# Optimization experiments

Hardware: AMD Instinct MI355X
Metric: run time of the kernel (lower is better)

Reference implementation:

```python
import jax, jax.numpy as jnp
import numpy as np

B, NF, NI = 4, 8, 1
C_ASPP = 512
H32, W32 = 32, 32
H8, W8 = 128, 128
C = C_ASPP // 16  # 32 channels after PixelShuffle(4)
D = 32 * 4 + 4 * 1 + 4 + 1  # 137 dynamic-kernel params per instance
BN_EPS = 1e-5


def pixel_shuffle(x, r):
    # torch PixelShuffle: out[n, c, h*r+i, w*r+j] = in[n, c*r*r + i*r + j, h, w]
    n, cr2, h, w = x.shape
    c = cr2 // (r * r)
    x = x.reshape(n, c, r, r, h, w)
    x = x.transpose(0, 1, 4, 2, 5, 3)
    return x.reshape(n, c, h * r, w * r)


def conv2d(x, w, b, pad):
    y = jax.lax.conv_general_dilated(
        x, w, window_strides=(1, 1), padding=[(pad, pad), (pad, pad)],
        dimension_numbers=("NCHW", "OIHW", "NCHW"))
    return y + b[None, :, None, None]


def setup_inputs() -> dict:
    key = jax.random.key(0)
    ks = jax.random.split(key, 6)
    return {
        "embedding": jax.random.normal(ks[0], (B * NF, C_ASPP, H32, W32), jnp.float32),
        "inc_kernels": jax.random.normal(ks[1], (B, NF, NI, D), jnp.float32) * 0.1,
        "coarse_masks": jax.random.uniform(ks[2], (B, NF, NI, H8, W8), dtype=jnp.float32),
        "conv_w": jax.random.normal(ks[3], (C, C, 3, 3), jnp.float32) * 0.05,
        "conv_b": jnp.zeros((C,), jnp.float32),
        "bn_gamma": jnp.ones((C,), jnp.float32),
        "bn_beta": jnp.zeros((C,), jnp.float32),
        "bn_mean": jnp.zeros((C,), jnp.float32),
        "bn_var": jnp.ones((C,), jnp.float32),
        "smooth_w": jax.random.normal(ks[4], (1, 2, 5, 5), jnp.float32) * 0.05,
        "smooth_b": jnp.zeros((1,), jnp.float32),
    }


def reference(embedding, inc_kernels, coarse_masks, conv_w, conv_b,
              bn_gamma, bn_beta, bn_mean, bn_var, smooth_w, smooth_b):
    # inc_conv: PixelShuffle(4) -> Conv3x3 -> BatchNorm(eval) -> ReLU
    x = pixel_shuffle(embedding, 4)              # (B*NF, 32, 128, 128)
    x = conv2d(x, conv_w, conv_b, 1)
    scale = (bn_gamma / jnp.sqrt(bn_var + BN_EPS))[None, :, None, None]
    x = (x - bn_mean[None, :, None, None]) * scale + bn_beta[None, :, None, None]
    x = jax.nn.relu(x)

    # per-instance dynamic 1x1 convs (groups = B*NF*NI; NI=1 so each frame is a group)
    G = B * NF * NI
    k = inc_kernels.reshape(G, D)
    w1 = k[:, :128].reshape(G, 4, 32)            # layer1: 32 -> 4
    w2 = k[:, 128:132].reshape(G, 1, 4)          # layer2: 4 -> 1
    b1 = k[:, 132:136]
    b2 = k[:, 136:137]

    hfeat = jax.nn.relu(jnp.einsum('goc,gchw->gohw', w1, x) + b1[:, :, None, None])
    y = jnp.einsum('goc,gchw->gohw', w2, hfeat) + b2[:, :, None, None]  # (G,1,H8,W8)

    m = coarse_masks.reshape(G, 1, H8, W8)
    z = jnp.concatenate([jax.nn.sigmoid(y), m], axis=1)  # (G, 2, H8, W8)
    z = conv2d(z, smooth_w, smooth_b, 2)                 # inc_smooth 5x5
    return z.reshape(B * NF, NI, H8, W8)
```

## Files before the change

kernel.cpp:

```cpp
#include <hip/hip_runtime.h>


typedef __attribute__((ext_vector_type(8))) short short8;
typedef __attribute__((ext_vector_type(4))) float f32x4;

static __device__ __forceinline__ ushort f2bf(float x) {
    union { float f; uint u; } v; v.f = x;
    uint r = v.u + 0x7fffu + ((v.u >> 16) & 1u);
    return (ushort)(r >> 16);
}
static __device__ __forceinline__ uint cvt_pk_bf16(float lo, float hi) {
    uint r;
    asm("v_cvt_pk_bf16_f32 %0, %1, %2" : "=v"(r) : "v"(lo), "v"(hi));
    return r;
}

#define SIG_ELEMS (32 * 128 * 128)
#define BFRAG_OFF (SIG_ELEMS * 4)
#define SH_OFF    (BFRAG_OFF + 18432)
#define HDP_OFF   (SH_OFF + 128)

__global__ void prep_kernel(const float* __restrict__ conv_w,
                            const float* __restrict__ conv_b,
                            const float* __restrict__ bn_gamma,
                            const float* __restrict__ bn_beta,
                            const float* __restrict__ bn_mean,
                            const float* __restrict__ bn_var,
                            const float* __restrict__ inc,
                            ushort* __restrict__ bfrag,
                            float* __restrict__ shb,
                            float* __restrict__ hdp) {
    int t = blockIdx.x * 256 + threadIdx.x;
    if (t < 9216) {
        int j    = t & 7;
        int lane = (t >> 3) & 63;
        int knt  = t >> 9;
        int kk   = knt >> 1;
        int nt   = knt & 1;
        int oc   = (lane & 15) + nt * 16;
        int c    = (lane >> 4) * 8 + j;
        float sc = bn_gamma[oc] * rsqrtf(bn_var[oc] + 1e-5f);
        bfrag[t] = f2bf(conv_w[oc * 288 + c * 9 + kk] * sc);
    } else if (t < 9248) {
        int oc = t - 9216;
        float sc = bn_gamma[oc] * rsqrtf(bn_var[oc] + 1e-5f);
        shb[oc] = (conv_b[oc] - bn_mean[oc]) * sc + bn_beta[oc];
    } else if (t < 9248 + 32 * 137) {
        int i = t - 9248;
        int nn = i / 137, r = i - nn * 137;
        hdp[nn * 144 + r] = inc[i];
    }
}

#define PITCHB 8320
#define NRING  6

__global__ __launch_bounds__(256, 2) void fused_main_kernel(
    const float* __restrict__ emb,
    const ushort* __restrict__ bfrag,
    const float* __restrict__ shb,
    const float* __restrict__ hdp,
    float* __restrict__ sig_out)
{
    __shared__ __align__(16) char smem[NRING * PITCHB];

    const int bid = blockIdx.x;
    const int lid = (bid & 7) * 64 + (bid >> 3);
    const int n   = lid >> 4;
    const int q   = lid & 15;
    const int hq0 = q << 3;

    const int tid  = threadIdx.x;

    const int f    = tid & 7;
    const int cphi = (tid >> 3) & 3;
    const int sx   = (tid >> 5) & 3;
    const int yy   = tid >> 7;

    {
        const int rA = yy, rB = yy + 2;
        const int hA = hq0 + rA - 1, hB = hq0 + rB - 1;
        const bool vA = (unsigned)hA < 128u;
        const bool vB = (unsigned)hB < 128u;
        float4 pA0[4], pA1[4], pB0[4], pB1[4];
        #pragma unroll
        for (int cplo = 0; cplo < 4; ++cplo) {
            pA0[cplo] = make_float4(0.f, 0.f, 0.f, 0.f);
            pA1[cplo] = pA0[cplo]; pB0[cplo] = pA0[cplo]; pB1[cplo] = pA0[cplo];
            if (vA) {
                int cc = cphi * 128 + cplo * 32 + ((hA & 3) << 2) + sx;
                long base = ((long)(n * 512 + cc) << 10) + ((hA >> 2) << 5) + (f << 2);
                pA0[cplo] = *reinterpret_cast<const float4*>(&emb[base]);
                pA1[cplo] = *reinterpret_cast<const float4*>(&emb[base + (16 << 10)]);
            }
            if (vB) {
                int cc = cphi * 128 + cplo * 32 + ((hB & 3) << 2) + sx;
                long base = ((long)(n * 512 + cc) << 10) + ((hB >> 2) << 5) + (f << 2);
                pB0[cplo] = *reinterpret_cast<const float4*>(&emb[base]);
                pB1[cplo] = *reinterpret_cast<const float4*>(&emb[base + (16 << 10)]);
            }
        }
        __builtin_amdgcn_sched_barrier(0);
        if (tid < 192) {
            int cell = tid >> 4;
            int wrd  = tid & 15;
            int row  = cell >> 1;
            int col  = (cell & 1) ? 129 : 0;
            ((uint*)smem)[(row * PITCHB + col * 64) / 4 + wrd] = 0u;
        }
        const float a00[4] = {pA0[0].x, pA0[0].y, pA0[0].z, pA0[0].w};
        const float a01[4] = {pA0[1].x, pA0[1].y, pA0[1].z, pA0[1].w};
        const float a02[4] = {pA0[2].x, pA0[2].y, pA0[2].z, pA0[2].w};
        const float a03[4] = {pA0[3].x, pA0[3].y, pA0[3].z, pA0[3].w};
        const float a10[4] = {pA1[0].x, pA1[0].y, pA1[0].z, pA1[0].w};
        const float a11[4] = {pA1[1].x, pA1[1].y, pA1[1].z, pA1[1].w};
        const float a12[4] = {pA1[2].x, pA1[2].y, pA1[2].z, pA1[2].w};
        const float a13[4] = {pA1[3].x, pA1[3].y, pA1[3].z, pA1[3].w};
        const float b00[4] = {pB0[0].x, pB0[0].y, pB0[0].z, pB0[0].w};
        const float b01[4] = {pB0[1].x, pB0[1].y, pB0[1].z, pB0[1].w};
        const float b02[4] = {pB0[2].x, pB0[2].y, pB0[2].z, pB0[2].w};
        const float b03[4] = {pB0[3].x, pB0[3].y, pB0[3].z, pB0[3].w};
        const float b10[4] = {pB1[0].x, pB1[0].y, pB1[0].z, pB1[0].w};
        const float b11[4] = {pB1[1].x, pB1[1].y, pB1[1].z, pB1[1].w};
        const float b12[4] = {pB1[2].x, pB1[2].y, pB1[2].z, pB1[2].w};
        const float b13[4] = {pB1[3].x, pB1[3].y, pB1[3].z, pB1[3].w};
        #pragma unroll
        for (int e = 0; e < 4; ++e) {
            int xi   = 1 + sx + (f << 4) + (e << 2);
            int slot = (cphi ^ ((xi >> 1) ^ (xi >> 4))) & 3;
            int off  = xi * 64 + (slot << 4);
            uint4 qa;
            qa.x = cvt_pk_bf16(a00[e], a10[e]);
            qa.y = cvt_pk_bf16(a01[e], a11[e]);
            qa.z = cvt_pk_bf16(a02[e], a12[e]);
            qa.w = cvt_pk_bf16(a03[e], a13[e]);
            *reinterpret_cast<uint4*>(&smem[rA * PITCHB + off]) = qa;
            uint4 qb;
            qb.x = cvt_pk_bf16(b00[e], b10[e]);
            qb.y = cvt_pk_bf16(b01[e], b11[e]);
            qb.z = cvt_pk_bf16(b02[e], b12[e]);
            qb.w = cvt_pk_bf16(b03[e], b13[e]);
            *reinterpret_cast<uint4*>(&smem[rB * PITCHB + off]) = qb;
        }
    }

    const int lane = tid & 63;
    const int wv   = tid >> 6;
    const int g    = lane >> 4;
    const int m    = lane & 15;
    const int rw   = wv >> 1;
    const int xq   = (wv & 1) * 64;

    int cell_off[4][3];
    #pragma unroll
    for (int t = 0; t < 4; ++t)
        #pragma unroll
        for (int dx = 0; dx < 3; ++dx) {
            int xi = xq + t * 16 + m + dx;
            int slot = (g ^ ((xi >> 1) ^ (xi >> 4))) & 3;
            cell_off[t][dx] = xi * 64 + (slot << 4);
        }

    short8 bf0[9], bf1[9];
    #pragma unroll
    for (int kk = 0; kk < 9; ++kk) {
        bf0[kk] = *reinterpret_cast<const short8*>(bfrag + (((kk * 2 + 0) * 64 + lane) << 3));
        bf1[kk] = *reinterpret_cast<const short8*>(bfrag + (((kk * 2 + 1) * 64 + lane) << 3));
    }

    const float* hd = hdp + n * 144;
    const f32x4 shA = *reinterpret_cast<const f32x4*>(&shb[g * 4]);
    const f32x4 shB = *reinterpret_cast<const f32x4*>(&shb[16 + g * 4]);
    f32x4 w1A[4], w1B[4];
    #pragma unroll
    for (int o = 0; o < 4; ++o) {
        w1A[o] = *reinterpret_cast<const f32x4*>(&hd[o * 32 + g * 4]);
        w1B[o] = *reinterpret_cast<const f32x4*>(&hd[o * 32 + 16 + g * 4]);
    }
    const f32x4 w2v = *reinterpret_cast<const f32x4*>(&hd[128]);
    const f32x4 b1v = *reinterpret_cast<const f32x4*>(&hd[132]);
    const float b2  = hd[136];

    __syncthreads();

    #pragma unroll 1
    for (int it = 0; it < 4; ++it) {
        float4 np0[4], np1[4];
        const bool have = (it < 3);
        const int  hn   = hq0 + 2 * it + 3 + yy;
        const bool vn   = have && (hn < 128);
        #pragma unroll
        for (int cplo = 0; cplo < 4; ++cplo) {
            np0[cplo] = make_float4(0.f, 0.f, 0.f, 0.f);
            np1[cplo] = np0[cplo];
            if (vn) {
                int cc = cphi * 128 + cplo * 32 + ((hn & 3) << 2) + sx;
                long base = ((long)(n * 512 + cc) << 10) + ((hn >> 2) << 5) + (f << 2);
                np0[cplo] = *reinterpret_cast<const float4*>(&emb[base]);
                np1[cplo] = *reinterpret_cast<const float4*>(&emb[base + (16 << 10)]);
            }
        }
        __builtin_amdgcn_sched_barrier(0);

        int rb[3];
        #pragma unroll
        for (int dy = 0; dy < 3; ++dy) {
            int r = 2 * it + rw + dy;
            if (r >= NRING) r -= NRING;
            rb[dy] = r * PITCHB;
        }

        f32x4 acc[4][2];
        #pragma unroll
        for (int t = 0; t < 4; ++t)
            #pragma unroll
            for (int nt = 0; nt < 2; ++nt)
                acc[t][nt] = (f32x4){0.f, 0.f, 0.f, 0.f};

        __builtin_amdgcn_s_setprio(1);
        #pragma unroll
        for (int kk = 0; kk < 9; ++kk) {
            const int dy = kk / 3, dxs = kk % 3;
            #pragma unroll
            for (int t = 0; t < 4; ++t) {
                short8 a = *reinterpret_cast<const short8*>(&smem[rb[dy] + cell_off[t][dxs]]);
                acc[t][0] = __builtin_amdgcn_mfma_f32_16x16x32_bf16(bf0[kk], a, acc[t][0], 0, 0, 0);
                acc[t][1] = __builtin_amdgcn_mfma_f32_16x16x32_bf16(bf1[kk], a, acc[t][1], 0, 0, 0);
            }
        }
        __builtin_amdgcn_s_setprio(0);

        float ph[4][4];
        #pragma unroll
        for (int t = 0; t < 4; ++t) {
            f32x4 vA, vB;
            vA.x = fmaxf(acc[t][0].x + shA.x, 0.f);
            vA.y = fmaxf(acc[t][0].y + shA.y, 0.f);
            vA.z = fmaxf(acc[t][0].z + shA.z, 0.f);
            vA.w = fmaxf(acc[t][0].w + shA.w, 0.f);
            vB.x = fmaxf(acc[t][1].x + shB.x, 0.f);
            vB.y = fmaxf(acc[t][1].y + shB.y, 0.f);
            vB.z = fmaxf(acc[t][1].z + shB.z, 0.f);
            vB.w = fmaxf(acc[t][1].w + shB.w, 0.f);
            #pragma unroll
            for (int o = 0; o < 4; ++o) {
                float p = vA.x * w1A[o].x;
                p = fmaf(vA.y, w1A[o].y, p);
                p = fmaf(vA.z, w1A[o].z, p);
                p = fmaf(vA.w, w1A[o].w, p);
                p = fmaf(vB.x, w1B[o].x, p);
                p = fmaf(vB.y, w1B[o].y, p);
                p = fmaf(vB.z, w1B[o].z, p);
                p = fmaf(vB.w, w1B[o].w, p);
                ph[t][o] = p;
            }
        }
        #pragma unroll
        for (int t = 0; t < 4; ++t)
            #pragma unroll
            for (int o = 0; o < 4; ++o) {
                float s = ph[t][o];
                s += __shfl_xor(s, 16);
                s += __shfl_xor(s, 32);
                ph[t][o] = s;
            }
        float yv[4];
        #pragma unroll
        for (int t = 0; t < 4; ++t) {
            float q0 = fmaxf(ph[t][0] + b1v.x, 0.f);
            float q1 = fmaxf(ph[t][1] + b1v.y, 0.f);
            float q2 = fmaxf(ph[t][2] + b1v.z, 0.f);
            float q3 = fmaxf(ph[t][3] + b1v.w, 0.f);
            float yyv = b2;
            yyv = fmaf(w2v.x, q0, yyv);
            yyv = fmaf(w2v.y, q1, yyv);
            yyv = fmaf(w2v.z, q2, yyv);
            yyv = fmaf(w2v.w, q3, yyv);
            yv[t] = yyv;
        }
        float ysel = (g == 0) ? yv[0] : (g == 1) ? yv[1] : (g == 2) ? yv[2] : yv[3];
        float sv = 1.0f / (1.0f + __expf(-ysel));
        sig_out[(n << 14) + ((hq0 + 2 * it + rw) << 7) + xq + lane] = sv;

        if (have) {
            int rs = 2 * it + 4 + yy;
            if (rs >= NRING) rs -= NRING;
            const float c00[4] = {np0[0].x, np0[0].y, np0[0].z, np0[0].w};
            const float c01[4] = {np0[1].x, np0[1].y, np0[1].z, np0[1].w};
            const float c02[4] = {np0[2].x, np0[2].y, np0[2].z, np0[2].w};
            const float c03[4] = {np0[3].x, np0[3].y, np0[3].z, np0[3].w};
            const float c10[4] = {np1[0].x, np1[0].y, np1[0].z, np1[0].w};
            const float c11[4] = {np1[1].x, np1[1].y, np1[1].z, np1[1].w};
            const float c12[4] = {np1[2].x, np1[2].y, np1[2].z, np1[2].w};
            const float c13[4] = {np1[3].x, np1[3].y, np1[3].z, np1[3].w};
            #pragma unroll
            for (int e = 0; e < 4; ++e) {
                int xi   = 1 + sx + (f << 4) + (e << 2);
                int slot = (cphi ^ ((xi >> 1) ^ (xi >> 4))) & 3;
                uint4 qv;
                qv.x = cvt_pk_bf16(c00[e], c10[e]);
                qv.y = cvt_pk_bf16(c01[e], c11[e]);
                qv.z = cvt_pk_bf16(c02[e], c12[e]);
                qv.w = cvt_pk_bf16(c03[e], c13[e]);
                *reinterpret_cast<uint4*>(&smem[rs * PITCHB + xi * 64 + (slot << 4)]) = qv;
            }
        }
        __syncthreads();
    }
}

__global__ __launch_bounds__(256) void smooth_kernel(
    const float* __restrict__ sig,
    const float* __restrict__ masks,
    const float* __restrict__ sw,
    const float* __restrict__ sb,
    float* __restrict__ out)
{
    __shared__ float ls[2][400];

    const int tid  = threadIdx.x;
    const int n    = blockIdx.x >> 6;
    const int tile = blockIdx.x & 63;
    const int h0   = (tile >> 3) << 4;
    const int w0   = (tile & 7) << 4;

    for (int i = tid; i < 800; i += 256) {
        int chn = (i >= 400) ? 1 : 0;
        int r  = i - chn * 400;
        int yy = r / 20;
        int xx = r - yy * 20;
        int h  = h0 + yy - 2;
        int w  = w0 + xx - 2;
        float v = 0.0f;
        if ((unsigned)h < 128u && (unsigned)w < 128u) {
            const float* src = chn ? masks : sig;
            v = src[(n << 14) + (h << 7) + w];
        }
        ls[chn][r] = v;
    }
    __syncthreads();

    const int tx = tid & 15;
    const int ty = tid >> 4;

    float accv = sb[0];
    #pragma unroll
    for (int chn = 0; chn < 2; ++chn)
        #pragma unroll
        for (int dy = 0; dy < 5; ++dy)
            #pragma unroll
            for (int dx = 0; dx < 5; ++dx)
                accv = fmaf(ls[chn][(ty + dy) * 20 + tx + dx],
                            sw[(chn * 5 + dy) * 5 + dx], accv);
    out[(n << 14) + ((h0 + ty) << 7) + (w0 + tx)] = accv;
}

extern "C" void kernel_launch(void* const* d_in, const int* in_sizes, int n_in,
                              void* d_out, int out_size, void* d_ws, size_t ws_size,
                              hipStream_t stream) {
    const float* emb     = (const float*)d_in[0];
    const float* inc     = (const float*)d_in[1];
    const float* masks   = (const float*)d_in[2];
    const float* conv_w  = (const float*)d_in[3];
    const float* conv_b  = (const float*)d_in[4];
    const float* bn_g    = (const float*)d_in[5];
    const float* bn_b    = (const float*)d_in[6];
    const float* bn_m    = (const float*)d_in[7];
    const float* bn_v    = (const float*)d_in[8];
    const float* sw      = (const float*)d_in[9];
    const float* sb      = (const float*)d_in[10];
    float*  out   = (float*)d_out;
    float*  sig   = (float*)d_ws;
    ushort* bfrag = (ushort*)((char*)d_ws + BFRAG_OFF);
    float*  shb   = (float*)((char*)d_ws + SH_OFF);
    float*  hdp   = (float*)((char*)d_ws + HDP_OFF);

    prep_kernel<<<54, 256, 0, stream>>>(conv_w, conv_b, bn_g, bn_b, bn_m, bn_v,
                                        inc, bfrag, shb, hdp);
    fused_main_kernel<<<512, 256, 0, stream>>>(emb, bfrag, shb, hdp, sig);
    smooth_kernel<<<2048, 256, 0, stream>>>(sig, masks, sw, sb, out);
}
```

Baseline: 33.91 us.

## Halve rows per block, double grid, raise occupancy and cut shuffle reduction

Each block now handles 4 output rows instead of 8, so the grid doubles to 1024 blocks, and launch bounds allow 3 blocks per CU. The thread-to-load mapping is permuted so consecutive threads vary sx and cphi first. The per-pixel weight and shift loads move inside the loop to reduce register pressure. The cross-lane reduction becomes a butterfly exchange, cutting the shuffle count. The cost is a larger relative halo: each 4-row strip still loads 6 input rows, so redundant global reads and conversion work go up.

```diff
diff --git a/kernel.cpp b/kernel.cpp
--- a/kernel.cpp
+++ b/kernel.cpp
@@ -55,7 +55,7 @@
 #define PITCHB 8320
 #define NRING  6
 
-__global__ __launch_bounds__(256, 2) void fused_main_kernel(
+__global__ __launch_bounds__(256, 3) void fused_main_kernel(
     const float* __restrict__ emb,
     const ushort* __restrict__ bfrag,
     const float* __restrict__ shb,
@@ -65,16 +65,16 @@
     __shared__ __align__(16) char smem[NRING * PITCHB];
 
     const int bid = blockIdx.x;
-    const int lid = (bid & 7) * 64 + (bid >> 3);
-    const int n   = lid >> 4;
-    const int q   = lid & 15;
-    const int hq0 = q << 3;
+    const int lid = (bid & 7) * 128 + (bid >> 3);
+    const int n   = lid >> 5;
+    const int qc  = lid & 31;
+    const int hq0 = qc << 2;
 
     const int tid  = threadIdx.x;
 
-    const int f    = tid & 7;
-    const int cphi = (tid >> 3) & 3;
-    const int sx   = (tid >> 5) & 3;
+    const int sx   = tid & 3;
+    const int cphi = (tid >> 2) & 3;
+    const int f    = (tid >> 4) & 7;
     const int yy   = tid >> 7;
 
     {
@@ -150,6 +150,8 @@
     const int m    = lane & 15;
     const int rw   = wv >> 1;
     const int xq   = (wv & 1) * 64;
+    const int gb0  = g & 1;
+    const int gb1  = (g >> 1) & 1;
 
     int cell_off[4][3];
     #pragma unroll
@@ -169,14 +171,6 @@
     }
 
     const float* hd = hdp + n * 144;
-    const f32x4 shA = *reinterpret_cast<const f32x4*>(&shb[g * 4]);
-    const f32x4 shB = *reinterpret_cast<const f32x4*>(&shb[16 + g * 4]);
-    f32x4 w1A[4], w1B[4];
-    #pragma unroll
-    for (int o = 0; o < 4; ++o) {
-        w1A[o] = *reinterpret_cast<const f32x4*>(&hd[o * 32 + g * 4]);
-        w1B[o] = *reinterpret_cast<const f32x4*>(&hd[o * 32 + 16 + g * 4]);
-    }
     const f32x4 w2v = *reinterpret_cast<const f32x4*>(&hd[128]);
     const f32x4 b1v = *reinterpret_cast<const f32x4*>(&hd[132]);
     const float b2  = hd[136];
@@ -184,9 +178,9 @@
     __syncthreads();
 
     #pragma unroll 1
-    for (int it = 0; it < 4; ++it) {
+    for (int it = 0; it < 2; ++it) {
         float4 np0[4], np1[4];
-        const bool have = (it < 3);
+        const bool have = (it == 0);
         const int  hn   = hq0 + 2 * it + 3 + yy;
         const bool vn   = have && (hn < 128);
         #pragma unroll
@@ -204,11 +198,8 @@
 
         int rb[3];
         #pragma unroll
-        for (int dy = 0; dy < 3; ++dy) {
-            int r = 2 * it + rw + dy;
-            if (r >= NRING) r -= NRING;
-            rb[dy] = r * PITCHB;
-        }
+        for (int dy = 0; dy < 3; ++dy)
+            rb[dy] = (2 * it + rw + dy) * PITCHB;
 
         f32x4 acc[4][2];
         #pragma unroll
@@ -229,6 +220,15 @@
             }
         }
         __builtin_amdgcn_s_setprio(0);
+
+        const f32x4 shA = *reinterpret_cast<const f32x4*>(&shb[g * 4]);
+        const f32x4 shB = *reinterpret_cast<const f32x4*>(&shb[16 + g * 4]);
+        f32x4 w1A[4], w1B[4];
+        #pragma unroll
+        for (int o = 0; o < 4; ++o) {
+            w1A[o] = *reinterpret_cast<const f32x4*>(&hd[o * 32 + g * 4]);
+            w1B[o] = *reinterpret_cast<const f32x4*>(&hd[o * 32 + 16 + g * 4]);
+        }
 
         float ph[4][4];
         #pragma unroll
@@ -255,36 +255,38 @@
                 ph[t][o] = p;
             }
         }
-        #pragma unroll
-        for (int t = 0; t < 4; ++t)
-            #pragma unroll
-            for (int o = 0; o < 4; ++o) {
-                float s = ph[t][o];
-                s += __shfl_xor(s, 16);
-                s += __shfl_xor(s, 32);
-                ph[t][o] = s;
-            }
-        float yv[4];
-        #pragma unroll
-        for (int t = 0; t < 4; ++t) {
-            float q0 = fmaxf(ph[t][0] + b1v.x, 0.f);
-            float q1 = fmaxf(ph[t][1] + b1v.y, 0.f);
-            float q2 = fmaxf(ph[t][2] + b1v.z, 0.f);
-            float q3 = fmaxf(ph[t][3] + b1v.w, 0.f);
-            float yyv = b2;
-            yyv = fmaf(w2v.x, q0, yyv);
-            yyv = fmaf(w2v.y, q1, yyv);
-            yyv = fmaf(w2v.z, q2, yyv);
-            yyv = fmaf(w2v.w, q3, yyv);
-            yv[t] = yyv;
-        }
-        float ysel = (g == 0) ? yv[0] : (g == 1) ? yv[1] : (g == 2) ? yv[2] : yv[3];
-        float sv = 1.0f / (1.0f + __expf(-ysel));
+
+        float k0[4], k1[4], tot[4];
+        #pragma unroll
+        for (int o = 0; o < 4; ++o) {
+            float send0 = gb0 ? ph[0][o] : ph[1][o];
+            float r0 = __shfl_xor(send0, 16);
+            k0[o] = (gb0 ? ph[1][o] : ph[0][o]) + r0;
+            float send1 = gb0 ? ph[2][o] : ph[3][o];
+            float r1 = __shfl_xor(send1, 16);
+            k1[o] = (gb0 ? ph[3][o] : ph[2][o]) + r1;
+        }
+        #pragma unroll
+        for (int o = 0; o < 4; ++o) {
+            float send = gb1 ? k0[o] : k1[o];
+            float r = __shfl_xor(send, 32);
+            tot[o] = (gb1 ? k1[o] : k0[o]) + r;
+        }
+
+        float q0 = fmaxf(tot[0] + b1v.x, 0.f);
+        float q1 = fmaxf(tot[1] + b1v.y, 0.f);
+        float q2 = fmaxf(tot[2] + b1v.z, 0.f);
+        float q3 = fmaxf(tot[3] + b1v.w, 0.f);
+        float yv = b2;
+        yv = fmaf(w2v.x, q0, yv);
+        yv = fmaf(w2v.y, q1, yv);
+        yv = fmaf(w2v.z, q2, yv);
+        yv = fmaf(w2v.w, q3, yv);
+        float sv = 1.0f / (1.0f + __expf(-yv));
         sig_out[(n << 14) + ((hq0 + 2 * it + rw) << 7) + xq + lane] = sv;
 
         if (have) {
-            int rs = 2 * it + 4 + yy;
-            if (rs >= NRING) rs -= NRING;
+            int rs = 4 + yy;
             const float c00[4] = {np0[0].x, np0[0].y, np0[0].z, np0[0].w};
             const float c01[4] = {np0[1].x, np0[1].y, np0[1].z, np0[1].w};
             const float c02[4] = {np0[2].x, np0[2].y, np0[2].z, np0[2].w};
@@ -377,6 +379,6 @@
 
     prep_kernel<<<54, 256, 0, stream>>>(conv_w, conv_b, bn_g, bn_b, bn_m, bn_v,
                                         inc, bfrag, shb, hdp);
-    fused_main_kernel<<<512, 256, 0, stream>>>(emb, bfrag, shb, hdp, sig);
+    fused_main_kernel<<<1024, 256, 0, stream>>>(emb, bfrag, shb, hdp, sig);
     smooth_kernel<<<2048, 256, 0, stream>>>(sig, masks, sw, sb, out);
 }
```

New measurement: 74.86 us. 121% more time.
